# Optimization experiments

Hardware: AMD Instinct MI355X
Metric: run time of the kernel (lower is better)

The kernel has to match this reference:

```python
import jax, jax.numpy as jnp
import numpy as np

HEADS = 16
EMBED = 1024
HEAD_DIM = EMBED // HEADS


def setup_inputs() -> dict:
    key = jax.random.key(0)
    ks = jax.random.split(key, 10)
    B, SQ, SKV = 2, 2048, 2048
    s = 1.0 / np.sqrt(HEAD_DIM)
    sd = 1.0 / np.sqrt(EMBED)
    return {
        "queries": jax.random.normal(ks[0], (B, SQ, EMBED), jnp.float32),
        "values": jax.random.normal(ks[1], (B, SKV, EMBED), jnp.float32),
        "heads": HEADS,
        "Wv": jax.random.normal(ks[2], (HEAD_DIM, HEAD_DIM), jnp.float32) * s,
        "bv": jax.random.normal(ks[3], (HEAD_DIM,), jnp.float32) * 0.02,
        "Wk": jax.random.normal(ks[4], (HEAD_DIM, HEAD_DIM), jnp.float32) * s,
        "bk": jax.random.normal(ks[5], (HEAD_DIM,), jnp.float32) * 0.02,
        "Wq": jax.random.normal(ks[6], (HEAD_DIM, HEAD_DIM), jnp.float32) * s,
        "bq": jax.random.normal(ks[7], (HEAD_DIM,), jnp.float32) * 0.02,
        "Wd": jax.random.normal(ks[8], (EMBED, EMBED), jnp.float32) * sd,
        "bd": jax.random.normal(ks[9], (EMBED,), jnp.float32) * 0.02,
    }


def reference(queries, values, heads, Wv, bv, Wk, bk, Wq, bq, Wd, bd):
    n, sq, e = queries.shape
    skv = values.shape[1]
    d = e // heads
    # reshape to per-head layout [b, s, h, d]
    q_in = queries.reshape(n, sq, heads, d)
    v_in = values.reshape(n, skv, heads, d)
    # shared per-head linear projections (torch Linear: x @ W.T + b)
    v = jnp.einsum("bshd,ed->bshe", v_in, Wv) + bv
    # quirk preserved: keys computed from the ALREADY-PROJECTED values
    k = jnp.einsum("bshd,ed->bshe", v, Wk) + bk
    q = jnp.einsum("bshd,ed->bshe", q_in, Wq) + bq
    # full O(n^2) score matrix [b, h, sq, skv] (as in source)
    scores = jnp.einsum("bqhd,bkhd->bhqk", q, k) / jnp.sqrt(jnp.asarray(d, q.dtype))
    attn = jax.nn.softmax(scores, axis=-1)
    out = jnp.einsum("bhqk,bkhd->bqhd", attn, v).reshape(n, sq, e)
    return out @ Wd.T + bd
```

## Files before the change

### kernel.cpp

```cpp
#include <hip/hip_runtime.h>
#include <hip/hip_bf16.h>
#include <hip/hip_fp16.h>
#include <math.h>

typedef _Float16 f16;
typedef _Float16 f16x8 __attribute__((ext_vector_type(8)));
typedef _Float16 f16x4 __attribute__((ext_vector_type(4)));
typedef _Float16 f16x2 __attribute__((ext_vector_type(2)));
typedef unsigned short u16x8v __attribute__((ext_vector_type(8)));
typedef float f32x4 __attribute__((ext_vector_type(4)));

namespace {
constexpr int B = 2;
constexpr int H = 16;
constexpr int S = 2048;
constexpr int D = 64;
constexpr int E = 1024;
constexpr float QSCALE = 0.125f * 1.4426950408889634f;
}

#define GLOBAL_LOAD_LDS16(gp, lp)                                              \
  __builtin_amdgcn_global_load_lds(                                            \
      (const __attribute__((address_space(1))) void*)(gp),                     \
      (__attribute__((address_space(3))) void*)(lp), 16, 0, 0)

__global__ __launch_bounds__(256) void prep(const float* __restrict__ Wd, f16* __restrict__ wd16,
                                            const float* __restrict__ Wk, const float* __restrict__ Wv,
                                            const float* __restrict__ bv, const float* __restrict__ bk,
                                            float* __restrict__ Wkv, float* __restrict__ bkv) {
  if (blockIdx.x < 1024) {
    const int i = blockIdx.x * 256 + threadIdx.x;
    const float4 f = ((const float4*)Wd)[i];
    f16x4 o;
    o.x = (f16)f.x; o.y = (f16)f.y; o.z = (f16)f.z; o.w = (f16)f.w;
    *(f16x4*)(wd16 + 4 * (size_t)i) = o;
  } else {
    const int g = (blockIdx.x - 1024) * 256 + threadIdx.x;
    const int i = g >> 6, j = g & 63;
    float s = 0.f;
#pragma unroll 16
    for (int d = 0; d < 64; ++d) s = fmaf(Wk[i * 64 + d], Wv[d * 64 + j], s);
    Wkv[g] = s;
    if (g < 64) {
      float bb = bk[g];
#pragma unroll 16
      for (int d = 0; d < 64; ++d) bb = fmaf(Wk[g * 64 + d], bv[d], bb);
      bkv[g] = bb;
    }
  }
}

__global__ __launch_bounds__(256) void proj3_mfma(const float* __restrict__ xq,
                                                  const float* __restrict__ xv,
                                                  const float* __restrict__ Wq,
                                                  const float* __restrict__ bq,
                                                  const float* __restrict__ Wv,
                                                  const float* __restrict__ bv,
                                                  const float* __restrict__ Wkv,
                                                  const float* __restrict__ bkv,
                                                  f16* __restrict__ qp,
                                                  f16* __restrict__ vtp,
                                                  f16* __restrict__ kp) {
  __shared__ f16 tb[16 * 16 * 68];
  const int which = blockIdx.y;
  const float* x = which ? xv : xq;

  const int t = threadIdx.x, lane = t & 63, w = t >> 6;
  const int l15 = lane & 15, quad = lane >> 4;
  const int m0 = (blockIdx.x * 4 + w) * 64;

  f16x8 af[4][2];
#pragma unroll
  for (int mt = 0; mt < 4; ++mt)
#pragma unroll
    for (int kc = 0; kc < 2; ++kc) {
      const float* g = x + (size_t)(m0 + mt * 16 + l15) * 64 + kc * 32 + quad * 8;
      const float4 a = *(const float4*)g, b2 = *(const float4*)(g + 4);
      f16x8 v;
      v[0]=(f16)a.x; v[1]=(f16)a.y; v[2]=(f16)a.z; v[3]=(f16)a.w;
      v[4]=(f16)b2.x; v[5]=(f16)b2.y; v[6]=(f16)b2.z; v[7]=(f16)b2.w;
      af[mt][kc] = v;
    }

  const int npass = which ? 2 : 1;
  for (int pass = 0; pass < npass; ++pass) {
    const float* W    = which ? (pass ? Wkv : Wv) : Wq;
    const float* bias = which ? (pass ? bkv : bv) : bq;
    const bool vpass  = (which == 1) && (pass == 0);
    const bool kpass  = (which == 1) && (pass == 1);
    const float scale = which ? 1.0f : QSCALE;

    f16x8 wf[4][2];
#pragma unroll
    for (int nt = 0; nt < 4; ++nt)
#pragma unroll
      for (int kc = 0; kc < 2; ++kc) {
        const float* g = W + (size_t)(nt * 16 + l15) * 64 + kc * 32 + quad * 8;
        const float4 a = *(const float4*)g, b2 = *(const float4*)(g + 4);
        f16x8 v;
        v[0]=(f16)a.x; v[1]=(f16)a.y; v[2]=(f16)a.z; v[3]=(f16)a.w;
        v[4]=(f16)b2.x; v[5]=(f16)b2.y; v[6]=(f16)b2.z; v[7]=(f16)b2.w;
        wf[nt][kc] = v;
      }

    f32x4 acc[4][4];
#pragma unroll
    for (int nt = 0; nt < 4; ++nt)
#pragma unroll
      for (int mt = 0; mt < 4; ++mt) acc[nt][mt] = (f32x4){0.f, 0.f, 0.f, 0.f};
#pragma unroll
    for (int kc = 0; kc < 2; ++kc)
#pragma unroll
      for (int nt = 0; nt < 4; ++nt)
#pragma unroll
        for (int mt = 0; mt < 4; ++mt)
          acc[nt][mt] = __builtin_amdgcn_mfma_f32_16x16x32_f16(wf[nt][kc], af[mt][kc], acc[nt][mt], 0, 0, 0);

    float4 bl4[4];
#pragma unroll
    for (int nt = 0; nt < 4; ++nt) bl4[nt] = *(const float4*)&bias[nt * 16 + quad * 4];

#pragma unroll
    for (int mt = 0; mt < 4; ++mt) {
      const int g = m0 + mt * 16 + l15;
#pragma unroll
      for (int nt = 0; nt < 4; ++nt) {
        const float p0 = (acc[nt][mt][0] + bl4[nt].x) * scale;
        const float p1 = (acc[nt][mt][1] + bl4[nt].y) * scale;
        const float p2 = (acc[nt][mt][2] + bl4[nt].z) * scale;
        const float p3 = (acc[nt][mt][3] + bl4[nt].w) * scale;
        union { f16x4 v4; f16x2 hh[2]; } u;
        u.hh[0] = __builtin_bit_cast(f16x2, __builtin_amdgcn_cvt_pkrtz(p0, p1));
        u.hh[1] = __builtin_bit_cast(f16x2, __builtin_amdgcn_cvt_pkrtz(p2, p3));
        if (vpass) {
#pragma unroll
          for (int r = 0; r < 4; ++r)
            tb[(l15 * 64 + nt * 16 + quad * 4 + r) * 16 + w * 4 + mt] = u.v4[r];
        } else if (kpass) {
          *(f16x4*)&tb[(l15 * 16 + w * 4 + mt) * 68 + nt * 16 + quad * 4] = u.v4;
        } else {
          *(f16x4*)(qp + (size_t)g * 64 + nt * 16 + quad * 4) = u.v4;
        }
      }
    }

    if (vpass) {
      __syncthreads();
      const int bsb = blockIdx.x * 16;
      const int bb = bsb >> 11;
      const int sb = bsb & 2047;
      const int off = sb & 63;
      const int poff = (off & 32) | ((off & 16) >> 2);
      const int col0 = (sb - off) + poff;
#pragma unroll
      for (int k2 = 0; k2 < 4; ++k2) {
        const int pi = t * 4 + k2;
        const int h = pi >> 6, d = pi & 63;
        const f16x8 lo = *(const f16x8*)&tb[pi * 16];
        const f16x8 hi = *(const f16x8*)&tb[pi * 16 + 8];
        f16* orow = vtp + ((size_t)(bb * H + h) * 64 + d) * S + col0;
        f16x4 g0, g1, g2, g3;
#pragma unroll
        for (int j = 0; j < 4; ++j) { g0[j]=lo[j]; g1[j]=lo[4+j]; g2[j]=hi[j]; g3[j]=hi[4+j]; }
        *(f16x4*)(orow + 0)  = g0;
        *(f16x4*)(orow + 8)  = g1;
        *(f16x4*)(orow + 16) = g2;
        *(f16x4*)(orow + 24) = g3;
      }
      __syncthreads();
    } else if (kpass) {
      __syncthreads();
      const int bsb = blockIdx.x * 16;
      const int bb = bsb >> 11;
      const int sblk = bsb & 2047;
      const int h = t >> 4, sl = t & 15;
      f16* dst = kp + ((size_t)(bb * H + h) * S + sblk + sl) * 64;
      const f16* src = &tb[t * 68];
#pragma unroll
      for (int c = 0; c < 8; ++c)
        *(f16x8*)(dst + c * 8) = *(const f16x8*)(src + c * 8);
    }
  }
}

__global__ __launch_bounds__(256) void attn_mfma(const f16* __restrict__ qp,
                                                 const f16* __restrict__ kp,
                                                 const f16* __restrict__ vtp,
                                                 f16* __restrict__ ao) {
  __shared__ f16 ks[2][128 * 64];
  __shared__ f16 vs[2][64 * 128];
  const int t = threadIdx.x, lane = t & 63, w = t >> 6;
  const int l15 = lane & 15, quad = lane >> 4;
  const int bh = blockIdx.x;
  const int b = bh >> 4, h = bh & 15;
  const int q0 = blockIdx.y * 128;
  const f16* kbase = kp + (size_t)bh * S * D;
  const f16* vtbase = vtp + (size_t)bh * 64 * S;

  const int c1 = w * 64 + lane;
  const int krow = c1 >> 3;
  const size_t koff1 = (size_t)krow * D + (((c1 & 7) ^ (krow & 7)) * 8);
  const int vrow = c1 >> 4;
  const size_t voff1 = (size_t)vrow * S + (((c1 & 15) ^ (vrow & 15)) * 8);

  f16x8 qf[2][2];
#pragma unroll
  for (int mt = 0; mt < 2; ++mt)
#pragma unroll
    for (int kc = 0; kc < 2; ++kc)
      qf[mt][kc] = *(const f16x8*)(qp +
          ((size_t)(b * S + q0 + w * 32 + mt * 16 + l15) * H + h) * 64 + kc * 32 + quad * 8);

  f16x8 vb4;
#pragma unroll
  for (int j = 0; j < 8; ++j) vb4[j] = (l15 == 0) ? (f16)1.0f : (f16)0.0f;

  f32x4 O[2][5];
#pragma unroll
  for (int mt = 0; mt < 2; ++mt)
#pragma unroll
    for (int nt = 0; nt < 5; ++nt) O[mt][nt] = (f32x4){0.f, 0.f, 0.f, 0.f};

#define ISSUE_TILE(tt, buf)                                                    \
  {                                                                            \
    const f16* gk = kbase + (size_t)(tt) * (128 * D);                          \
    _Pragma("unroll")                                                          \
    for (int i = 0; i < 4; ++i)                                                \
      GLOBAL_LOAD_LDS16(gk + koff1 + (size_t)i * (32 * D),                     \
                        &ks[buf][(i * 256 + w * 64) * 8]);                     \
    const f16* gv = vtbase + (size_t)(tt) * 128;                               \
    _Pragma("unroll")                                                          \
    for (int i = 0; i < 4; ++i)                                                \
      GLOBAL_LOAD_LDS16(gv + voff1 + (size_t)i * (16 * S),                     \
                        &vs[buf][(i * 256 + w * 64) * 8]);                     \
  }

  ISSUE_TILE(0, 0);

  for (int kt = 0; kt < S / 128; ++kt) {
    const int rb = kt & 1;
    __asm__ volatile("s_waitcnt vmcnt(0)" ::: "memory");
    __builtin_amdgcn_s_barrier();
    __asm__ volatile("" ::: "memory");
    if (kt + 1 < S / 128) ISSUE_TILE(kt + 1, rb ^ 1);

#pragma unroll
    for (int kc = 0; kc < 4; ++kc) {
      f32x4 sc[2][2];
#pragma unroll
      for (int ntl = 0; ntl < 2; ++ntl)
#pragma unroll
        for (int mt = 0; mt < 2; ++mt) sc[ntl][mt] = (f32x4){0.f, 0.f, 0.f, 0.f};
      __builtin_amdgcn_s_setprio(1);
#pragma unroll
      for (int kcq = 0; kcq < 2; ++kcq)
#pragma unroll
        for (int ntl = 0; ntl < 2; ++ntl) {
          const int nt = kc * 2 + ntl;
          const f16x8 kf = *(const f16x8*)&ks[rb][(nt * 16 + l15) * 64 + (((kcq * 4 + quad) ^ (l15 & 7)) * 8)];
#pragma unroll
          for (int mt = 0; mt < 2; ++mt)
            sc[ntl][mt] = __builtin_amdgcn_mfma_f32_16x16x32_f16(kf, qf[mt][kcq], sc[ntl][mt], 0, 0, 0);
        }
      __builtin_amdgcn_s_setprio(0);

      f16x8 pa[2];
#pragma unroll
      for (int mt = 0; mt < 2; ++mt) {
        const f32x4 s0 = sc[0][mt], s1 = sc[1][mt];
        union { f16x8 v8; f16x2 hh[4]; } u;
        u.hh[0] = __builtin_bit_cast(f16x2, __builtin_amdgcn_cvt_pkrtz(
            __builtin_amdgcn_exp2f(s0[0]), __builtin_amdgcn_exp2f(s0[1])));
        u.hh[1] = __builtin_bit_cast(f16x2, __builtin_amdgcn_cvt_pkrtz(
            __builtin_amdgcn_exp2f(s0[2]), __builtin_amdgcn_exp2f(s0[3])));
        u.hh[2] = __builtin_bit_cast(f16x2, __builtin_amdgcn_cvt_pkrtz(
            __builtin_amdgcn_exp2f(s1[0]), __builtin_amdgcn_exp2f(s1[1])));
        u.hh[3] = __builtin_bit_cast(f16x2, __builtin_amdgcn_cvt_pkrtz(
            __builtin_amdgcn_exp2f(s1[2]), __builtin_amdgcn_exp2f(s1[3])));
        pa[mt] = u.v8;
      }

      __builtin_amdgcn_s_setprio(1);
#pragma unroll
      for (int nt = 0; nt < 4; ++nt) {
        const f16x8 vbf = *(const f16x8*)&vs[rb][(nt * 16 + l15) * 128 + (((kc * 4 + quad) ^ l15) * 8)];
#pragma unroll
        for (int mt = 0; mt < 2; ++mt)
          O[mt][nt] = __builtin_amdgcn_mfma_f32_16x16x32_f16(pa[mt], vbf, O[mt][nt], 0, 0, 0);
      }
#pragma unroll
      for (int mt = 0; mt < 2; ++mt)
        O[mt][4] = __builtin_amdgcn_mfma_f32_16x16x32_f16(pa[mt], vb4, O[mt][4], 0, 0, 0);
      __builtin_amdgcn_s_setprio(0);
    }
  }
#undef ISSUE_TILE

#pragma unroll
  for (int mt = 0; mt < 2; ++mt)
#pragma unroll
    for (int r = 0; r < 4; ++r) {
      const float l = __shfl(O[mt][4][r], quad << 4, 64);
      const float inv = 1.f / l;
      const int row = q0 + w * 32 + mt * 16 + quad * 4 + r;
      f16* o = ao + ((size_t)b * S + row) * E + h * D;
#pragma unroll
      for (int nt = 0; nt < 4; ++nt)
        o[nt * 16 + l15] = (f16)(O[mt][nt][r] * inv);
    }
}

__global__ __launch_bounds__(256) void dense_mfma(const f16* __restrict__ A,
                                                  const f16* __restrict__ Wd16,
                                                  const float* __restrict__ bd,
                                                  float* __restrict__ out) {
  __shared__ f16 as[3][128 * 64];
  __shared__ f16 bs[3][64 * 64];
  const int t = threadIdx.x;
  const int lane = t & 63;
  const int w = t >> 6;
  const int l15 = lane & 15;
  const int quad = lane >> 4;
  const int m0 = blockIdx.x * 128;
  const int n0 = blockIdx.y * 64;
  const int wm = (w >> 1) * 64, wn = (w & 1) * 32;

  const int srow = (lane >> 3);
  const int schunk = (lane & 7) ^ srow;
  const f16* ga0 = A    + (size_t)(m0 + w * 32 + srow) * E + schunk * 8;
  const f16* gb0 = Wd16 + (size_t)(n0 + w * 16 + srow) * E + schunk * 8;

  constexpr int NT = E / 64;

#define ISSUE_D(tt, ib)                                                        \
  {                                                                            \
    _Pragma("unroll")                                                          \
    for (int i = 0; i < 4; ++i)                                                \
      GLOBAL_LOAD_LDS16(ga0 + (size_t)(i * 8) * E + (tt) * 64,                 \
                        &as[ib][(w * 32 + i * 8) * 64]);                       \
    _Pragma("unroll")                                                          \
    for (int i = 0; i < 2; ++i)                                                \
      GLOBAL_LOAD_LDS16(gb0 + (size_t)(i * 8) * E + (tt) * 64,                 \
// ... 49 lines not shown
    for (int mt = 0; mt < 4; ++mt)
#pragma unroll
      for (int r = 0; r < 4; ++r)
        out[(size_t)(m0 + wm + mt * 16 + quad * 4 + r) * E + col] = acc[mt][nt][r] + bdv;
  }
}

extern "C" void kernel_launch(void* const* d_in, const int* in_sizes, int n_in,
                              void* d_out, int out_size, void* d_ws, size_t ws_size,
                              hipStream_t stream) {
  const float* queries = (const float*)d_in[0];
  const float* values  = (const float*)d_in[1];
  const float* Wv = (const float*)d_in[3];
  const float* bv = (const float*)d_in[4];
  const float* Wk = (const float*)d_in[5];
  const float* bk = (const float*)d_in[6];
  const float* Wq = (const float*)d_in[7];
  const float* bq = (const float*)d_in[8];
  const float* Wd = (const float*)d_in[9];
  const float* bd = (const float*)d_in[10];
  float* out = (float*)d_out;

  char* ws = (char*)d_ws;
  f16* qp    = (f16*)(ws);
  f16* kp    = (f16*)(ws + 8u * 1024 * 1024);
  f16* vtp   = (f16*)(ws + 16u * 1024 * 1024);
  f16* ao    = (f16*)(ws + 24u * 1024 * 1024);
  f16* wd16  = (f16*)(ws + 32u * 1024 * 1024);
  float* wkv = (float*)(ws + 34u * 1024 * 1024);
  float* bkv = (float*)(ws + 34u * 1024 * 1024 + 16384);
  (void)ws_size; (void)in_sizes; (void)n_in; (void)out_size;

  prep<<<1040, 256, 0, stream>>>(Wd, wd16, Wk, Wv, bv, bk, wkv, bkv);
  proj3_mfma<<<dim3(256, 2), 256, 0, stream>>>(queries, values, Wq, bq, Wv, bv, wkv, bkv, qp, vtp, kp);
  attn_mfma<<<dim3(B * H, S / 128), 256, 0, stream>>>(qp, kp, vtp, ao);
  dense_mfma<<<dim3(B * S / 128, E / 64), 256, 0, stream>>>(ao, wd16, bd, out);
}
```

Before: 177.7 us.

## Shrink attention tiles to 64 queries and 64 keys for higher occupancy

The attention kernel now uses 64-query blocks (16 rows per wave instead of 32) and 64-key tiles, halving LDS buffers and per-thread accumulators, and requests 4 blocks per CU via launch bounds. The grid doubles to 1024 blocks, which gives better CU fill and latency hiding on the device. In exchange, each K/V tile is reused by half as many queries, doubling global/L2 traffic for K and V, and there are twice as many barrier iterations per block.

```diff
diff --git a/kernel.cpp b/kernel.cpp
--- a/kernel.cpp
+++ b/kernel.cpp
@@ -183,74 +183,64 @@
   }
 }
 
-__global__ __launch_bounds__(256) void attn_mfma(const f16* __restrict__ qp,
-                                                 const f16* __restrict__ kp,
-                                                 const f16* __restrict__ vtp,
-                                                 f16* __restrict__ ao) {
-  __shared__ f16 ks[2][128 * 64];
-  __shared__ f16 vs[2][64 * 128];
+__global__ __launch_bounds__(256, 4) void attn_mfma(const f16* __restrict__ qp,
+                                                    const f16* __restrict__ kp,
+                                                    const f16* __restrict__ vtp,
+                                                    f16* __restrict__ ao) {
+  __shared__ f16 ks[2][64 * 64];
+  __shared__ f16 vs[2][64 * 64];
   const int t = threadIdx.x, lane = t & 63, w = t >> 6;
   const int l15 = lane & 15, quad = lane >> 4;
   const int bh = blockIdx.x;
   const int b = bh >> 4, h = bh & 15;
-  const int q0 = blockIdx.y * 128;
+  const int q0 = blockIdx.y * 64;
   const f16* kbase = kp + (size_t)bh * S * D;
   const f16* vtbase = vtp + (size_t)bh * 64 * S;
 
-  const int c1 = w * 64 + lane;
-  const int krow = c1 >> 3;
-  const size_t koff1 = (size_t)krow * D + (((c1 & 7) ^ (krow & 7)) * 8);
-  const int vrow = c1 >> 4;
-  const size_t voff1 = (size_t)vrow * S + (((c1 & 15) ^ (vrow & 15)) * 8);
-
-  f16x8 qf[2][2];
-#pragma unroll
-  for (int mt = 0; mt < 2; ++mt)
-#pragma unroll
-    for (int kc = 0; kc < 2; ++kc)
-      qf[mt][kc] = *(const f16x8*)(qp +
-          ((size_t)(b * S + q0 + w * 32 + mt * 16 + l15) * H + h) * 64 + kc * 32 + quad * 8);
+  const int row1 = t >> 3;
+  const size_t koff1 = (size_t)row1 * D + (((t & 7) ^ (row1 & 7)) * 8);
+  const size_t koff2 = koff1 + (size_t)32 * D;
+  const size_t voff1 = (size_t)row1 * S + (((t & 7) ^ (row1 & 7)) * 8);
+  const size_t voff2 = voff1 + (size_t)32 * S;
+
+  f16x8 qf[2];
+#pragma unroll
+  for (int kc = 0; kc < 2; ++kc)
+    qf[kc] = *(const f16x8*)(qp +
+        ((size_t)(b * S + q0 + w * 16 + l15) * H + h) * 64 + kc * 32 + quad * 8);
 
   f16x8 vb4;
 #pragma unroll
   for (int j = 0; j < 8; ++j) vb4[j] = (l15 == 0) ? (f16)1.0f : (f16)0.0f;
 
-  f32x4 O[2][5];
-#pragma unroll
-  for (int mt = 0; mt < 2; ++mt)
-#pragma unroll
-    for (int nt = 0; nt < 5; ++nt) O[mt][nt] = (f32x4){0.f, 0.f, 0.f, 0.f};
+  f32x4 O[5];
+#pragma unroll
+  for (int nt = 0; nt < 5; ++nt) O[nt] = (f32x4){0.f, 0.f, 0.f, 0.f};
 
 #define ISSUE_TILE(tt, buf)                                                    \
   {                                                                            \
-    const f16* gk = kbase + (size_t)(tt) * (128 * D);                          \
-    _Pragma("unroll")                                                          \
-    for (int i = 0; i < 4; ++i)                                                \
-      GLOBAL_LOAD_LDS16(gk + koff1 + (size_t)i * (32 * D),                     \
-                        &ks[buf][(i * 256 + w * 64) * 8]);                     \
-    const f16* gv = vtbase + (size_t)(tt) * 128;                               \
-    _Pragma("unroll")                                                          \
-    for (int i = 0; i < 4; ++i)                                                \
-      GLOBAL_LOAD_LDS16(gv + voff1 + (size_t)i * (16 * S),                     \
-                        &vs[buf][(i * 256 + w * 64) * 8]);                     \
+    const f16* gk = kbase + (size_t)(tt) * (64 * D);                           \
+    GLOBAL_LOAD_LDS16(gk + koff1, &ks[buf][t * 8]);                            \
+    GLOBAL_LOAD_LDS16(gk + koff2, &ks[buf][(t + 256) * 8]);                    \
+    const f16* gv = vtbase + (size_t)(tt) * 64;                                \
+    GLOBAL_LOAD_LDS16(gv + voff1, &vs[buf][t * 8]);                            \
+    GLOBAL_LOAD_LDS16(gv + voff2, &vs[buf][(t + 256) * 8]);                    \
   }
 
   ISSUE_TILE(0, 0);
 
-  for (int kt = 0; kt < S / 128; ++kt) {
+  for (int kt = 0; kt < S / 64; ++kt) {
     const int rb = kt & 1;
     __asm__ volatile("s_waitcnt vmcnt(0)" ::: "memory");
     __builtin_amdgcn_s_barrier();
     __asm__ volatile("" ::: "memory");
-    if (kt + 1 < S / 128) ISSUE_TILE(kt + 1, rb ^ 1);
-
-#pragma unroll
-    for (int kc = 0; kc < 4; ++kc) {
-      f32x4 sc[2][2];
-#pragma unroll
-      for (int ntl = 0; ntl < 2; ++ntl)
-#pragma unroll
-        for (int mt = 0; mt < 2; ++mt) sc[ntl][mt] = (f32x4){0.f, 0.f, 0.f, 0.f};
+    if (kt + 1 < S / 64) ISSUE_TILE(kt + 1, rb ^ 1);
+
+#pragma unroll
+    for (int kc = 0; kc < 2; ++kc) {
+      f32x4 sc[2];
+#pragma unroll
+      for (int ntl = 0; ntl < 2; ++ntl) sc[ntl] = (f32x4){0.f, 0.f, 0.f, 0.f};
       __builtin_amdgcn_s_setprio(1);
 #pragma unroll
       for (int kcq = 0; kcq < 2; ++kcq)
@@ -258,16 +248,13 @@
         for (int ntl = 0; ntl < 2; ++ntl) {
           const int nt = kc * 2 + ntl;
           const f16x8 kf = *(const f16x8*)&ks[rb][(nt * 16 + l15) * 64 + (((kcq * 4 + quad) ^ (l15 & 7)) * 8)];
-#pragma unroll
-          for (int mt = 0; mt < 2; ++mt)
-            sc[ntl][mt] = __builtin_amdgcn_mfma_f32_16x16x32_f16(kf, qf[mt][kcq], sc[ntl][mt], 0, 0, 0);
+          sc[ntl] = __builtin_amdgcn_mfma_f32_16x16x32_f16(kf, qf[kcq], sc[ntl], 0, 0, 0);
         }
       __builtin_amdgcn_s_setprio(0);
 
-      f16x8 pa[2];
-#pragma unroll
-      for (int mt = 0; mt < 2; ++mt) {
-        const f32x4 s0 = sc[0][mt], s1 = sc[1][mt];
+      f16x8 pa;
+      {
+        const f32x4 s0 = sc[0], s1 = sc[1];
         union { f16x8 v8; f16x2 hh[4]; } u;
         u.hh[0] = __builtin_bit_cast(f16x2, __builtin_amdgcn_cvt_pkrtz(
             __builtin_amdgcn_exp2f(s0[0]), __builtin_amdgcn_exp2f(s0[1])));
@@ -277,37 +264,31 @@
             __builtin_amdgcn_exp2f(s1[0]), __builtin_amdgcn_exp2f(s1[1])));
         u.hh[3] = __builtin_bit_cast(f16x2, __builtin_amdgcn_cvt_pkrtz(
             __builtin_amdgcn_exp2f(s1[2]), __builtin_amdgcn_exp2f(s1[3])));
-        pa[mt] = u.v8;
+        pa = u.v8;
       }
 
       __builtin_amdgcn_s_setprio(1);
 #pragma unroll
       for (int nt = 0; nt < 4; ++nt) {
-        const f16x8 vbf = *(const f16x8*)&vs[rb][(nt * 16 + l15) * 128 + (((kc * 4 + quad) ^ l15) * 8)];
-#pragma unroll
-        for (int mt = 0; mt < 2; ++mt)
-          O[mt][nt] = __builtin_amdgcn_mfma_f32_16x16x32_f16(pa[mt], vbf, O[mt][nt], 0, 0, 0);
-      }
-#pragma unroll
-      for (int mt = 0; mt < 2; ++mt)
-        O[mt][4] = __builtin_amdgcn_mfma_f32_16x16x32_f16(pa[mt], vb4, O[mt][4], 0, 0, 0);
+        const f16x8 vbf = *(const f16x8*)&vs[rb][(nt * 16 + l15) * 64 + (((kc * 4 + quad) ^ (l15 & 7)) * 8)];
+        O[nt] = __builtin_amdgcn_mfma_f32_16x16x32_f16(pa, vbf, O[nt], 0, 0, 0);
+      }
+      O[4] = __builtin_amdgcn_mfma_f32_16x16x32_f16(pa, vb4, O[4], 0, 0, 0);
       __builtin_amdgcn_s_setprio(0);
     }
   }
 #undef ISSUE_TILE
 
 #pragma unroll
-  for (int mt = 0; mt < 2; ++mt)
-#pragma unroll
-    for (int r = 0; r < 4; ++r) {
-      const float l = __shfl(O[mt][4][r], quad << 4, 64);
-      const float inv = 1.f / l;
-      const int row = q0 + w * 32 + mt * 16 + quad * 4 + r;
-      f16* o = ao + ((size_t)b * S + row) * E + h * D;
-#pragma unroll
-      for (int nt = 0; nt < 4; ++nt)
-        o[nt * 16 + l15] = (f16)(O[mt][nt][r] * inv);
-    }
+  for (int r = 0; r < 4; ++r) {
+    const float l = __shfl(O[4][r], quad << 4, 64);
+    const float inv = 1.f / l;
+    const int row = q0 + w * 16 + quad * 4 + r;
+    f16* o = ao + ((size_t)b * S + row) * E + h * D;
+#pragma unroll
+    for (int nt = 0; nt < 4; ++nt)
+      o[nt * 16 + l15] = (f16)(O[nt][r] * inv);
+  }
 }
 
 __global__ __launch_bounds__(256) void dense_mfma(const f16* __restrict__ A,
@@ -424,6 +405,6 @@
 
   prep<<<1040, 256, 0, stream>>>(Wd, wd16, Wk, Wv, bv, bk, wkv, bkv);
   proj3_mfma<<<dim3(256, 2), 256, 0, stream>>>(queries, values, Wq, bq, Wv, bv, wkv, bkv, qp, vtp, kp);
-  attn_mfma<<<dim3(B * H, S / 128), 256, 0, stream>>>(qp, kp, vtp, ao);
+  attn_mfma<<<dim3(B * H, S / 64), 256, 0, stream>>>(qp, kp, vtp, ao);
   dense_mfma<<<dim3(B * S / 128, E / 64), 256, 0, stream>>>(ao, wd16, bd, out);
 }
```

Result: no change. 180.6 us (+1.7%).

## Split KV across waves in attention and move V projection to its own kernel

Applied to the files above, without the earlier changes.

The attention kernel now uses 64-query blocks, twice as many blocks, and splits each 64-key tile across two wave pairs. Partial O and row-sum accumulators are combined through shared memory at the end. The V-transpose projection moves out of the fused projection kernel into a separate per-head kernel, leaving Q/K projection with a single pass. The aim is better occupancy and parallelism on the dominant attention stage, at the cost of an extra kernel launch and a final cross-wave reduction.

```diff
diff --git a/kernel.cpp b/kernel.cpp
--- a/kernel.cpp
+++ b/kernel.cpp
@@ -50,20 +50,20 @@
   }
 }
 
-__global__ __launch_bounds__(256) void proj3_mfma(const float* __restrict__ xq,
-                                                  const float* __restrict__ xv,
-                                                  const float* __restrict__ Wq,
-                                                  const float* __restrict__ bq,
-                                                  const float* __restrict__ Wv,
-                                                  const float* __restrict__ bv,
-                                                  const float* __restrict__ Wkv,
-                                                  const float* __restrict__ bkv,
-                                                  f16* __restrict__ qp,
-                                                  f16* __restrict__ vtp,
-                                                  f16* __restrict__ kp) {
+__global__ __launch_bounds__(256) void projqk_mfma(const float* __restrict__ xq,
+                                                   const float* __restrict__ xv,
+                                                   const float* __restrict__ Wq,
+                                                   const float* __restrict__ bq,
+                                                   const float* __restrict__ Wkv,
+                                                   const float* __restrict__ bkv,
+                                                   f16* __restrict__ qp,
+                                                   f16* __restrict__ kp) {
   __shared__ f16 tb[16 * 16 * 68];
   const int which = blockIdx.y;
-  const float* x = which ? xv : xq;
+  const float* x    = which ? xv : xq;
+  const float* W    = which ? Wkv : Wq;
+  const float* bias = which ? bkv : bq;
+  const float scale = which ? 1.0f : QSCALE;
 
   const int t = threadIdx.x, lane = t & 63, w = t >> 6;
   const int l15 = lane & 15, quad = lane >> 4;
@@ -82,126 +82,153 @@
       af[mt][kc] = v;
     }
 
-  const int npass = which ? 2 : 1;
-  for (int pass = 0; pass < npass; ++pass) {
-    const float* W    = which ? (pass ? Wkv : Wv) : Wq;
-    const float* bias = which ? (pass ? bkv : bv) : bq;
-    const bool vpass  = (which == 1) && (pass == 0);
-    const bool kpass  = (which == 1) && (pass == 1);
-    const float scale = which ? 1.0f : QSCALE;
-
-    f16x8 wf[4][2];
+  f16x8 wf[4][2];
+#pragma unroll
+  for (int nt = 0; nt < 4; ++nt)
+#pragma unroll
+    for (int kc = 0; kc < 2; ++kc) {
+      const float* g = W + (size_t)(nt * 16 + l15) * 64 + kc * 32 + quad * 8;
+      const float4 a = *(const float4*)g, b2 = *(const float4*)(g + 4);
+      f16x8 v;
+      v[0]=(f16)a.x; v[1]=(f16)a.y; v[2]=(f16)a.z; v[3]=(f16)a.w;
+      v[4]=(f16)b2.x; v[5]=(f16)b2.y; v[6]=(f16)b2.z; v[7]=(f16)b2.w;
+      wf[nt][kc] = v;
+    }
+
+  f32x4 acc[4][4];
+#pragma unroll
+  for (int nt = 0; nt < 4; ++nt)
+#pragma unroll
+    for (int mt = 0; mt < 4; ++mt) acc[nt][mt] = (f32x4){0.f, 0.f, 0.f, 0.f};
+#pragma unroll
+  for (int kc = 0; kc < 2; ++kc)
 #pragma unroll
     for (int nt = 0; nt < 4; ++nt)
 #pragma unroll
-      for (int kc = 0; kc < 2; ++kc) {
-        const float* g = W + (size_t)(nt * 16 + l15) * 64 + kc * 32 + quad * 8;
-        const float4 a = *(const float4*)g, b2 = *(const float4*)(g + 4);
-        f16x8 v;
-        v[0]=(f16)a.x; v[1]=(f16)a.y; v[2]=(f16)a.z; v[3]=(f16)a.w;
-        v[4]=(f16)b2.x; v[5]=(f16)b2.y; v[6]=(f16)b2.z; v[7]=(f16)b2.w;
-        wf[nt][kc] = v;
+      for (int mt = 0; mt < 4; ++mt)
+        acc[nt][mt] = __builtin_amdgcn_mfma_f32_16x16x32_f16(wf[nt][kc], af[mt][kc], acc[nt][mt], 0, 0, 0);
+
+  float4 bl4[4];
+#pragma unroll
+  for (int nt = 0; nt < 4; ++nt) bl4[nt] = *(const float4*)&bias[nt * 16 + quad * 4];
+
+#pragma unroll
+  for (int mt = 0; mt < 4; ++mt) {
+    const int g = m0 + mt * 16 + l15;
+#pragma unroll
+    for (int nt = 0; nt < 4; ++nt) {
+      const float p0 = (acc[nt][mt][0] + bl4[nt].x) * scale;
+      const float p1 = (acc[nt][mt][1] + bl4[nt].y) * scale;
+      const float p2 = (acc[nt][mt][2] + bl4[nt].z) * scale;
+      const float p3 = (acc[nt][mt][3] + bl4[nt].w) * scale;
+      union { f16x4 v4; f16x2 hh[2]; } u;
+      u.hh[0] = __builtin_bit_cast(f16x2, __builtin_amdgcn_cvt_pkrtz(p0, p1));
+      u.hh[1] = __builtin_bit_cast(f16x2, __builtin_amdgcn_cvt_pkrtz(p2, p3));
+      if (which) {
+        *(f16x4*)&tb[(l15 * 16 + w * 4 + mt) * 68 + nt * 16 + quad * 4] = u.v4;
+      } else {
+        *(f16x4*)(qp + (size_t)g * 64 + nt * 16 + quad * 4) = u.v4;
       }
-
-    f32x4 acc[4][4];
-#pragma unroll
-    for (int nt = 0; nt < 4; ++nt)
-#pragma unroll
-      for (int mt = 0; mt < 4; ++mt) acc[nt][mt] = (f32x4){0.f, 0.f, 0.f, 0.f};
-#pragma unroll
-    for (int kc = 0; kc < 2; ++kc)
-#pragma unroll
-      for (int nt = 0; nt < 4; ++nt)
-#pragma unroll
-        for (int mt = 0; mt < 4; ++mt)
-          acc[nt][mt] = __builtin_amdgcn_mfma_f32_16x16x32_f16(wf[nt][kc], af[mt][kc], acc[nt][mt], 0, 0, 0);
-
-    float4 bl4[4];
-#pragma unroll
-    for (int nt = 0; nt < 4; ++nt) bl4[nt] = *(const float4*)&bias[nt * 16 + quad * 4];
-
-#pragma unroll
-    for (int mt = 0; mt < 4; ++mt) {
-      const int g = m0 + mt * 16 + l15;
-#pragma unroll
-      for (int nt = 0; nt < 4; ++nt) {
-        const float p0 = (acc[nt][mt][0] + bl4[nt].x) * scale;
-        const float p1 = (acc[nt][mt][1] + bl4[nt].y) * scale;
-        const float p2 = (acc[nt][mt][2] + bl4[nt].z) * scale;
-        const float p3 = (acc[nt][mt][3] + bl4[nt].w) * scale;
-        union { f16x4 v4; f16x2 hh[2]; } u;
-        u.hh[0] = __builtin_bit_cast(f16x2, __builtin_amdgcn_cvt_pkrtz(p0, p1));
-        u.hh[1] = __builtin_bit_cast(f16x2, __builtin_amdgcn_cvt_pkrtz(p2, p3));
-        if (vpass) {
-#pragma unroll
-          for (int r = 0; r < 4; ++r)
-            tb[(l15 * 64 + nt * 16 + quad * 4 + r) * 16 + w * 4 + mt] = u.v4[r];
-        } else if (kpass) {
-          *(f16x4*)&tb[(l15 * 16 + w * 4 + mt) * 68 + nt * 16 + quad * 4] = u.v4;
-        } else {
-          *(f16x4*)(qp + (size_t)g * 64 + nt * 16 + quad * 4) = u.v4;
-        }
-      }
-    }
-
-    if (vpass) {
-      __syncthreads();
-      const int bsb = blockIdx.x * 16;
-      const int bb = bsb >> 11;
-      const int sb = bsb & 2047;
-      const int off = sb & 63;
-      const int poff = (off & 32) | ((off & 16) >> 2);
-      const int col0 = (sb - off) + poff;
-#pragma unroll
-      for (int k2 = 0; k2 < 4; ++k2) {
-        const int pi = t * 4 + k2;
-        const int h = pi >> 6, d = pi & 63;
-        const f16x8 lo = *(const f16x8*)&tb[pi * 16];
-        const f16x8 hi = *(const f16x8*)&tb[pi * 16 + 8];
-        f16* orow = vtp + ((size_t)(bb * H + h) * 64 + d) * S + col0;
-        f16x4 g0, g1, g2, g3;
-#pragma unroll
-        for (int j = 0; j < 4; ++j) { g0[j]=lo[j]; g1[j]=lo[4+j]; g2[j]=hi[j]; g3[j]=hi[4+j]; }
-        *(f16x4*)(orow + 0)  = g0;
-        *(f16x4*)(orow + 8)  = g1;
-        *(f16x4*)(orow + 16) = g2;
-        *(f16x4*)(orow + 24) = g3;
-      }
-      __syncthreads();
-    } else if (kpass) {
-      __syncthreads();
-      const int bsb = blockIdx.x * 16;
-      const int bb = bsb >> 11;
-      const int sblk = bsb & 2047;
-      const int h = t >> 4, sl = t & 15;
-      f16* dst = kp + ((size_t)(bb * H + h) * S + sblk + sl) * 64;
-      const f16* src = &tb[t * 68];
-#pragma unroll
-      for (int c = 0; c < 8; ++c)
-        *(f16x8*)(dst + c * 8) = *(const f16x8*)(src + c * 8);
-    }
-  }
-}
-
-__global__ __launch_bounds__(256) void attn_mfma(const f16* __restrict__ qp,
-                                                 const f16* __restrict__ kp,
-                                                 const f16* __restrict__ vtp,
-                                                 f16* __restrict__ ao) {
-  __shared__ f16 ks[2][128 * 64];
-  __shared__ f16 vs[2][64 * 128];
+    }
+  }
+
+  if (which) {
+    __syncthreads();
+    const int bsb = blockIdx.x * 16;
+    const int bb = bsb >> 11;
+    const int sblk = bsb & 2047;
+    const int h = t >> 4, sl = t & 15;
+    f16* dst = kp + ((size_t)(bb * H + h) * S + sblk + sl) * 64;
+    const f16* src = &tb[t * 68];
+#pragma unroll
+    for (int c = 0; c < 8; ++c)
+      *(f16x8*)(dst + c * 8) = *(const f16x8*)(src + c * 8);
+  }
+}
+
+__global__ __launch_bounds__(256) void projv_mfma(const float* __restrict__ xv,
+                                                  const float* __restrict__ Wv,
+                                                  const float* __restrict__ bv,
+                                                  f16* __restrict__ vtp) {
+  __shared__ f16 tb[64 * 72];
   const int t = threadIdx.x, lane = t & 63, w = t >> 6;
   const int l15 = lane & 15, quad = lane >> 4;
+  const int b = blockIdx.x >> 5, s0 = (blockIdx.x & 31) * 64;
+  const int h = blockIdx.y;
+
+  f16x8 af[2];
+#pragma unroll
+  for (int kc = 0; kc < 2; ++kc) {
+    const float* g = xv + ((size_t)(b * S + s0 + w * 16 + l15) * H + h) * 64 + kc * 32 + quad * 8;
+    const float4 a = *(const float4*)g, b2 = *(const float4*)(g + 4);
+    f16x8 v;
+    v[0]=(f16)a.x; v[1]=(f16)a.y; v[2]=(f16)a.z; v[3]=(f16)a.w;
+    v[4]=(f16)b2.x; v[5]=(f16)b2.y; v[6]=(f16)b2.z; v[7]=(f16)b2.w;
+    af[kc] = v;
+  }
+  f16x8 wf[4][2];
+#pragma unroll
+  for (int nt = 0; nt < 4; ++nt)
+#pragma unroll
+    for (int kc = 0; kc < 2; ++kc) {
+      const float* g = Wv + (size_t)(nt * 16 + l15) * 64 + kc * 32 + quad * 8;
+      const float4 a = *(const float4*)g, b2 = *(const float4*)(g + 4);
+      f16x8 v;
+      v[0]=(f16)a.x; v[1]=(f16)a.y; v[2]=(f16)a.z; v[3]=(f16)a.w;
+      v[4]=(f16)b2.x; v[5]=(f16)b2.y; v[6]=(f16)b2.z; v[7]=(f16)b2.w;
+      wf[nt][kc] = v;
+    }
+
+  f32x4 acc[4];
+#pragma unroll
+  for (int nt = 0; nt < 4; ++nt) acc[nt] = (f32x4){0.f, 0.f, 0.f, 0.f};
+#pragma unroll
+  for (int kc = 0; kc < 2; ++kc)
+#pragma unroll
+    for (int nt = 0; nt < 4; ++nt)
+      acc[nt] = __builtin_amdgcn_mfma_f32_16x16x32_f16(af[kc], wf[nt][kc], acc[nt], 0, 0, 0);
+
+  float bl[4];
+#pragma unroll
+  for (int nt = 0; nt < 4; ++nt) bl[nt] = bv[nt * 16 + l15];
+
+#pragma unroll
+  for (int nt = 0; nt < 4; ++nt)
+#pragma unroll
+    for (int r = 0; r < 4; ++r)
+      tb[(nt * 16 + l15) * 72 + w * 16 + quad * 4 + r] = (f16)(acc[nt][r] + bl[nt]);
+
+  __syncthreads();
+  const int d = t >> 2;
+  f16* orow = vtp + ((size_t)(b * H + h) * 64 + d) * S + s0;
+  const f16* src = &tb[d * 72];
+#pragma unroll
+  for (int j = 0; j < 4; ++j) {
+    const int g = (t & 3) * 4 + j;
+    const int p = ((g >> 3) & 1) * 32 + ((g >> 1) & 1) * 16 + (g & 1) * 8 + ((g >> 2) & 1) * 4;
+    *(f16x4*)(orow + p) = *(const f16x4*)(src + g * 4);
+  }
+}
+
+__global__ __launch_bounds__(256, 4) void attn_mfma(const f16* __restrict__ qp,
+                                                    const f16* __restrict__ kp,
+                                                    const f16* __restrict__ vtp,
+                                                    f16* __restrict__ ao) {
+  __shared__ f16 smem[4][64 * 64];
+  const int t = threadIdx.x, lane = t & 63, w = t >> 6;
+  const int l15 = lane & 15, quad = lane >> 4;
+  const int wq = w >> 1, wk = w & 1;
   const int bh = blockIdx.x;
   const int b = bh >> 4, h = bh & 15;
-  const int q0 = blockIdx.y * 128;
+  const int q0 = blockIdx.y * 64;
   const f16* kbase = kp + (size_t)bh * S * D;
   const f16* vtbase = vtp + (size_t)bh * 64 * S;
 
-  const int c1 = w * 64 + lane;
-  const int krow = c1 >> 3;
-  const size_t koff1 = (size_t)krow * D + (((c1 & 7) ^ (krow & 7)) * 8);
-  const int vrow = c1 >> 4;
-  const size_t voff1 = (size_t)vrow * S + (((c1 & 15) ^ (vrow & 15)) * 8);
+  const int row1 = t >> 3;
+  const size_t koff1 = (size_t)row1 * D + (((t & 7) ^ (row1 & 7)) * 8);
+  const size_t koff2 = koff1 + (size_t)32 * D;
+  const size_t voff1 = (size_t)row1 * S + (((t & 7) ^ (row1 & 7)) * 8);
+  const size_t voff2 = voff1 + (size_t)32 * S;
 
   f16x8 qf[2][2];
 #pragma unroll
@@ -209,7 +236,7 @@
 #pragma unroll
     for (int kc = 0; kc < 2; ++kc)
       qf[mt][kc] = *(const f16x8*)(qp +
-          ((size_t)(b * S + q0 + w * 32 + mt * 16 + l15) * H + h) * 64 + kc * 32 + quad * 8);
+          ((size_t)(b * S + q0 + wq * 32 + mt * 16 + l15) * H + h) * 64 + kc * 32 + quad * 8);
 
   f16x8 vb4;
 #pragma unroll
@@ -223,91 +250,104 @@
 
 #define ISSUE_TILE(tt, buf)                                                    \
   {                                                                            \
-    const f16* gk = kbase + (size_t)(tt) * (128 * D);                          \
-    _Pragma("unroll")                                                          \
-    for (int i = 0; i < 4; ++i)                                                \
-      GLOBAL_LOAD_LDS16(gk + koff1 + (size_t)i * (32 * D),                     \
-                        &ks[buf][(i * 256 + w * 64) * 8]);                     \
-    const f16* gv = vtbase + (size_t)(tt) * 128;                               \
-    _Pragma("unroll")                                                          \
-    for (int i = 0; i < 4; ++i)                                                \
-      GLOBAL_LOAD_LDS16(gv + voff1 + (size_t)i * (16 * S),                     \
-                        &vs[buf][(i * 256 + w * 64) * 8]);                     \
+    const f16* gk = kbase + (size_t)(tt) * (64 * D);                           \
+    GLOBAL_LOAD_LDS16(gk + koff1, &smem[buf][t * 8]);                          \
+    GLOBAL_LOAD_LDS16(gk + koff2, &smem[buf][(t + 256) * 8]);                  \
+    const f16* gv = vtbase + (size_t)(tt) * 64;                                \
+    GLOBAL_LOAD_LDS16(gv + voff1, &smem[2 + (buf)][t * 8]);                    \
+    GLOBAL_LOAD_LDS16(gv + voff2, &smem[2 + (buf)][(t + 256) * 8]);            \
   }
 
   ISSUE_TILE(0, 0);
 
-  for (int kt = 0; kt < S / 128; ++kt) {
+  for (int kt = 0; kt < S / 64; ++kt) {
     const int rb = kt & 1;
     __asm__ volatile("s_waitcnt vmcnt(0)" ::: "memory");
     __builtin_amdgcn_s_barrier();
     __asm__ volatile("" ::: "memory");
-    if (kt + 1 < S / 128) ISSUE_TILE(kt + 1, rb ^ 1);
-
-#pragma unroll
-    for (int kc = 0; kc < 4; ++kc) {
-      f32x4 sc[2][2];
-#pragma unroll
-      for (int ntl = 0; ntl < 2; ++ntl)
-#pragma unroll
-        for (int mt = 0; mt < 2; ++mt) sc[ntl][mt] = (f32x4){0.f, 0.f, 0.f, 0.f};
-      __builtin_amdgcn_s_setprio(1);
-#pragma unroll
-      for (int kcq = 0; kcq < 2; ++kcq)
-#pragma unroll
-        for (int ntl = 0; ntl < 2; ++ntl) {
-          const int nt = kc * 2 + ntl;
-          const f16x8 kf = *(const f16x8*)&ks[rb][(nt * 16 + l15) * 64 + (((kcq * 4 + quad) ^ (l15 & 7)) * 8)];
-#pragma unroll
-          for (int mt = 0; mt < 2; ++mt)
-            sc[ntl][mt] = __builtin_amdgcn_mfma_f32_16x16x32_f16(kf, qf[mt][kcq], sc[ntl][mt], 0, 0, 0);
-        }
-      __builtin_amdgcn_s_setprio(0);
-
-      f16x8 pa[2];
-#pragma unroll
-      for (int mt = 0; mt < 2; ++mt) {
-        const f32x4 s0 = sc[0][mt], s1 = sc[1][mt];
-        union { f16x8 v8; f16x2 hh[4]; } u;
-        u.hh[0] = __builtin_bit_cast(f16x2, __builtin_amdgcn_cvt_pkrtz(
-            __builtin_amdgcn_exp2f(s0[0]), __builtin_amdgcn_exp2f(s0[1])));
-        u.hh[1] = __builtin_bit_cast(f16x2, __builtin_amdgcn_cvt_pkrtz(
-            __builtin_amdgcn_exp2f(s0[2]), __builtin_amdgcn_exp2f(s0[3])));
-        u.hh[2] = __builtin_bit_cast(f16x2, __builtin_amdgcn_cvt_pkrtz(
-            __builtin_amdgcn_exp2f(s1[0]), __builtin_amdgcn_exp2f(s1[1])));
-        u.hh[3] = __builtin_bit_cast(f16x2, __builtin_amdgcn_cvt_pkrtz(
-            __builtin_amdgcn_exp2f(s1[2]), __builtin_amdgcn_exp2f(s1[3])));
-        pa[mt] = u.v8;
+    if (kt + 1 < S / 64) ISSUE_TILE(kt + 1, rb ^ 1);
+
+    f32x4 sc[2][2];
+#pragma unroll
+    for (int ntl = 0; ntl < 2; ++ntl)
+#pragma unroll
+      for (int mt = 0; mt < 2; ++mt) sc[ntl][mt] = (f32x4){0.f, 0.f, 0.f, 0.f};
+    __builtin_amdgcn_s_setprio(1);
+#pragma unroll
+    for (int kcq = 0; kcq < 2; ++kcq)
+#pragma unroll
+      for (int ntl = 0; ntl < 2; ++ntl) {
+        const f16x8 kf = *(const f16x8*)&smem[rb][(wk * 32 + ntl * 16 + l15) * 64 + (((kcq * 4 + quad) ^ (l15 & 7)) * 8)];
+#pragma unroll
+        for (int mt = 0; mt < 2; ++mt)
+          sc[ntl][mt] = __builtin_amdgcn_mfma_f32_16x16x32_f16(kf, qf[mt][kcq], sc[ntl][mt], 0, 0, 0);
       }
-
-      __builtin_amdgcn_s_setprio(1);
-#pragma unroll
-      for (int nt = 0; nt < 4; ++nt) {
-        const f16x8 vbf = *(const f16x8*)&vs[rb][(nt * 16 + l15) * 128 + (((kc * 4 + quad) ^ l15) * 8)];
-#pragma unroll
-        for (int mt = 0; mt < 2; ++mt)
-          O[mt][nt] = __builtin_amdgcn_mfma_f32_16x16x32_f16(pa[mt], vbf, O[mt][nt], 0, 0, 0);
+    __builtin_amdgcn_s_setprio(0);
+
+    f16x8 pa[2];
+#pragma unroll
+    for (int mt = 0; mt < 2; ++mt) {
+      const f32x4 s0 = sc[0][mt], s1 = sc[1][mt];
+      union { f16x8 v8; f16x2 hh[4]; } u;
+      u.hh[0] = __builtin_bit_cast(f16x2, __builtin_amdgcn_cvt_pkrtz(
+          __builtin_amdgcn_exp2f(s0[0]), __builtin_amdgcn_exp2f(s0[1])));
+      u.hh[1] = __builtin_bit_cast(f16x2, __builtin_amdgcn_cvt_pkrtz(
+          __builtin_amdgcn_exp2f(s0[2]), __builtin_amdgcn_exp2f(s0[3])));
+      u.hh[2] = __builtin_bit_cast(f16x2, __builtin_amdgcn_cvt_pkrtz(
+          __builtin_amdgcn_exp2f(s1[0]), __builtin_amdgcn_exp2f(s1[1])));
+      u.hh[3] = __builtin_bit_cast(f16x2, __builtin_amdgcn_cvt_pkrtz(
+          __builtin_amdgcn_exp2f(s1[2]), __builtin_amdgcn_exp2f(s1[3])));
+      pa[mt] = u.v8;
+    }
+
+    __builtin_amdgcn_s_setprio(1);
+#pragma unroll
+    for (int nt = 0; nt < 4; ++nt) {
+      const f16x8 vbf = *(const f16x8*)&smem[2 + rb][(nt * 16 + l15) * 64 + (((wk * 4 + quad) ^ (l15 & 7)) * 8)];
+#pragma unroll
+      for (int mt = 0; mt < 2; ++mt)
+        O[mt][nt] = __builtin_amdgcn_mfma_f32_16x16x32_f16(pa[mt], vbf, O[mt][nt], 0, 0, 0);
+    }
+#pragma unroll
+    for (int mt = 0; mt < 2; ++mt)
+      O[mt][4] = __builtin_amdgcn_mfma_f32_16x16x32_f16(pa[mt], vb4, O[mt][4], 0, 0, 0);
+    __builtin_amdgcn_s_setprio(0);
+  }
+#undef ISSUE_TILE
+
+  __syncthreads();
+  float* red = (float*)&smem[0][0];
+  if (wk) {
+    float* dst = red + (size_t)(wq * 64 + lane) * 41;
+#pragma unroll
+    for (int mt = 0; mt < 2; ++mt)
+#pragma unroll
+      for (int nt = 0; nt < 5; ++nt)
+#pragma unroll
+        for (int r = 0; r < 4; ++r) dst[mt * 20 + nt * 4 + r] = O[mt][nt][r];
+  }
+  __syncthreads();
+  if (!wk) {
+    const float* src = red + (size_t)(wq * 64 + lane) * 41;
+#pragma unroll
+    for (int mt = 0; mt < 2; ++mt)
+#pragma unroll
+      for (int nt = 0; nt < 5; ++nt)
+#pragma unroll
+        for (int r = 0; r < 4; ++r) O[mt][nt][r] += src[mt * 20 + nt * 4 + r];
+#pragma unroll
+    for (int mt = 0; mt < 2; ++mt)
+#pragma unroll
+      for (int r = 0; r < 4; ++r) {
+        const float l = __shfl(O[mt][4][r], quad << 4, 64);
+        const float inv = 1.f / l;
+        const int row = q0 + wq * 32 + mt * 16 + quad * 4 + r;
+        f16* o = ao + ((size_t)b * S + row) * E + h * D;
+#pragma unroll
+        for (int nt = 0; nt < 4; ++nt)
+          o[nt * 16 + l15] = (f16)(O[mt][nt][r] * inv);
       }
-#pragma unroll
-      for (int mt = 0; mt < 2; ++mt)
-        O[mt][4] = __builtin_amdgcn_mfma_f32_16x16x32_f16(pa[mt], vb4, O[mt][4], 0, 0, 0);
-      __builtin_amdgcn_s_setprio(0);
-    }
-  }
-#undef ISSUE_TILE
-
-#pragma unroll
-  for (int mt = 0; mt < 2; ++mt)
-#pragma unroll
-    for (int r = 0; r < 4; ++r) {
-      const float l = __shfl(O[mt][4][r], quad << 4, 64);
-      const float inv = 1.f / l;
-      const int row = q0 + w * 32 + mt * 16 + quad * 4 + r;
-      f16* o = ao + ((size_t)b * S + row) * E + h * D;
-#pragma unroll
-      for (int nt = 0; nt < 4; ++nt)
-        o[nt * 16 + l15] = (f16)(O[mt][nt][r] * inv);
-    }
+  }
 }
 
 __global__ __launch_bounds__(256) void dense_mfma(const f16* __restrict__ A,
@@ -423,7 +463,8 @@
   (void)ws_size; (void)in_sizes; (void)n_in; (void)out_size;
 
   prep<<<1040, 256, 0, stream>>>(Wd, wd16, Wk, Wv, bv, bk, wkv, bkv);
-  proj3_mfma<<<dim3(256, 2), 256, 0, stream>>>(queries, values, Wq, bq, Wv, bv, wkv, bkv, qp, vtp, kp);
-  attn_mfma<<<dim3(B * H, S / 128), 256, 0, stream>>>(qp, kp, vtp, ao);
+  projqk_mfma<<<dim3(256, 2), 256, 0, stream>>>(queries, values, Wq, bq, wkv, bkv, qp, kp);
+  projv_mfma<<<dim3(B * S / 64, H), 256, 0, stream>>>(values, Wv, bv, vtp);
+  attn_mfma<<<dim3(B * H, S / 64), 256, 0, stream>>>(qp, kp, vtp, ao);
   dense_mfma<<<dim3(B * S / 128, E / 64), 256, 0, stream>>>(ao, wd16, bd, out);
 }
```

New measurement: 179.3 us. Within noise of the previous version (+0.9%).

## Split attention KV dimension across wave pairs with LDS reduction, 512 threads

Applied to the files above, without the earlier changes.

The attention kernel now uses 512 threads per block. Each pair of waves shares a 32-row query slab and splits each 64-key tile between them, so each block runs 8 waves. The KV tile shrinks from 128 to 64 keys to cut LDS to 32 KB, allowing more blocks per CU. Partial O and row-sum accumulators are combined through LDS at the end, which adds a few barriers and extra LDS traffic. The aim is more waves in flight to hide latency, at the cost of twice as many loop iterations and barriers.

```diff
diff --git a/kernel.cpp b/kernel.cpp
--- a/kernel.cpp
+++ b/kernel.cpp
@@ -183,25 +183,23 @@
   }
 }
 
-__global__ __launch_bounds__(256) void attn_mfma(const f16* __restrict__ qp,
-                                                 const f16* __restrict__ kp,
-                                                 const f16* __restrict__ vtp,
-                                                 f16* __restrict__ ao) {
-  __shared__ f16 ks[2][128 * 64];
-  __shared__ f16 vs[2][64 * 128];
+__global__ __launch_bounds__(512, 4) void attn_mfma(const f16* __restrict__ qp,
+                                                    const f16* __restrict__ kp,
+                                                    const f16* __restrict__ vtp,
+                                                    f16* __restrict__ ao) {
+  __shared__ f16 smem[4][64 * 64];
   const int t = threadIdx.x, lane = t & 63, w = t >> 6;
   const int l15 = lane & 15, quad = lane >> 4;
+  const int wq = w >> 1, wk = w & 1;
   const int bh = blockIdx.x;
   const int b = bh >> 4, h = bh & 15;
   const int q0 = blockIdx.y * 128;
   const f16* kbase = kp + (size_t)bh * S * D;
   const f16* vtbase = vtp + (size_t)bh * 64 * S;
 
-  const int c1 = w * 64 + lane;
-  const int krow = c1 >> 3;
-  const size_t koff1 = (size_t)krow * D + (((c1 & 7) ^ (krow & 7)) * 8);
-  const int vrow = c1 >> 4;
-  const size_t voff1 = (size_t)vrow * S + (((c1 & 15) ^ (vrow & 15)) * 8);
+  const int row1 = t >> 3;
+  const size_t koff = (size_t)row1 * D + (((t & 7) ^ (row1 & 7)) * 8);
+  const size_t voff = (size_t)row1 * S + (((t & 7) ^ (row1 & 7)) * 8);
 
   f16x8 qf[2][2];
 #pragma unroll
@@ -209,7 +207,7 @@
 #pragma unroll
     for (int kc = 0; kc < 2; ++kc)
       qf[mt][kc] = *(const f16x8*)(qp +
-          ((size_t)(b * S + q0 + w * 32 + mt * 16 + l15) * H + h) * 64 + kc * 32 + quad * 8);
+          ((size_t)(b * S + q0 + wq * 32 + mt * 16 + l15) * H + h) * 64 + kc * 32 + quad * 8);
 
   f16x8 vb4;
 #pragma unroll
@@ -223,91 +221,115 @@
 
 #define ISSUE_TILE(tt, buf)                                                    \
   {                                                                            \
-    const f16* gk = kbase + (size_t)(tt) * (128 * D);                          \
-    _Pragma("unroll")                                                          \
-    for (int i = 0; i < 4; ++i)                                                \
-      GLOBAL_LOAD_LDS16(gk + koff1 + (size_t)i * (32 * D),                     \
-                        &ks[buf][(i * 256 + w * 64) * 8]);                     \
-    const f16* gv = vtbase + (size_t)(tt) * 128;                               \
-    _Pragma("unroll")                                                          \
-    for (int i = 0; i < 4; ++i)                                                \
-      GLOBAL_LOAD_LDS16(gv + voff1 + (size_t)i * (16 * S),                     \
-                        &vs[buf][(i * 256 + w * 64) * 8]);                     \
+    const f16* gk = kbase + (size_t)(tt) * (64 * D);                           \
+    GLOBAL_LOAD_LDS16(gk + koff, &smem[buf][t * 8]);                           \
+    const f16* gv = vtbase + (size_t)(tt) * 64;                                \
+    GLOBAL_LOAD_LDS16(gv + voff, &smem[2 + (buf)][t * 8]);                     \
   }
 
   ISSUE_TILE(0, 0);
 
-  for (int kt = 0; kt < S / 128; ++kt) {
+  for (int kt = 0; kt < S / 64; ++kt) {
     const int rb = kt & 1;
     __asm__ volatile("s_waitcnt vmcnt(0)" ::: "memory");
     __builtin_amdgcn_s_barrier();
     __asm__ volatile("" ::: "memory");
-    if (kt + 1 < S / 128) ISSUE_TILE(kt + 1, rb ^ 1);
-
-#pragma unroll
-    for (int kc = 0; kc < 4; ++kc) {
-      f32x4 sc[2][2];
-#pragma unroll
-      for (int ntl = 0; ntl < 2; ++ntl)
-#pragma unroll
-        for (int mt = 0; mt < 2; ++mt) sc[ntl][mt] = (f32x4){0.f, 0.f, 0.f, 0.f};
-      __builtin_amdgcn_s_setprio(1);
-#pragma unroll
-      for (int kcq = 0; kcq < 2; ++kcq)
-#pragma unroll
-        for (int ntl = 0; ntl < 2; ++ntl) {
-          const int nt = kc * 2 + ntl;
-          const f16x8 kf = *(const f16x8*)&ks[rb][(nt * 16 + l15) * 64 + (((kcq * 4 + quad) ^ (l15 & 7)) * 8)];
-#pragma unroll
-          for (int mt = 0; mt < 2; ++mt)
-            sc[ntl][mt] = __builtin_amdgcn_mfma_f32_16x16x32_f16(kf, qf[mt][kcq], sc[ntl][mt], 0, 0, 0);
-        }
-      __builtin_amdgcn_s_setprio(0);
-
-      f16x8 pa[2];
-#pragma unroll
-      for (int mt = 0; mt < 2; ++mt) {
-        const f32x4 s0 = sc[0][mt], s1 = sc[1][mt];
-        union { f16x8 v8; f16x2 hh[4]; } u;
-        u.hh[0] = __builtin_bit_cast(f16x2, __builtin_amdgcn_cvt_pkrtz(
-            __builtin_amdgcn_exp2f(s0[0]), __builtin_amdgcn_exp2f(s0[1])));
-        u.hh[1] = __builtin_bit_cast(f16x2, __builtin_amdgcn_cvt_pkrtz(
-            __builtin_amdgcn_exp2f(s0[2]), __builtin_amdgcn_exp2f(s0[3])));
-        u.hh[2] = __builtin_bit_cast(f16x2, __builtin_amdgcn_cvt_pkrtz(
-            __builtin_amdgcn_exp2f(s1[0]), __builtin_amdgcn_exp2f(s1[1])));
-        u.hh[3] = __builtin_bit_cast(f16x2, __builtin_amdgcn_cvt_pkrtz(
-            __builtin_amdgcn_exp2f(s1[2]), __builtin_amdgcn_exp2f(s1[3])));
-        pa[mt] = u.v8;
-      }
-
-      __builtin_amdgcn_s_setprio(1);
-#pragma unroll
-      for (int nt = 0; nt < 4; ++nt) {
-        const f16x8 vbf = *(const f16x8*)&vs[rb][(nt * 16 + l15) * 128 + (((kc * 4 + quad) ^ l15) * 8)];
+    if (kt + 1 < S / 64) ISSUE_TILE(kt + 1, rb ^ 1);
+
+    f32x4 sc[2][2];
+#pragma unroll
+    for (int ntl = 0; ntl < 2; ++ntl)
+#pragma unroll
+      for (int mt = 0; mt < 2; ++mt) sc[ntl][mt] = (f32x4){0.f, 0.f, 0.f, 0.f};
+    __builtin_amdgcn_s_setprio(1);
+#pragma unroll
+    for (int kcq = 0; kcq < 2; ++kcq)
+#pragma unroll
+      for (int ntl = 0; ntl < 2; ++ntl) {
+        const f16x8 kf = *(const f16x8*)&smem[rb][(wk * 32 + ntl * 16 + l15) * 64 + (((kcq * 4 + quad) ^ (l15 & 7)) * 8)];
 #pragma unroll
         for (int mt = 0; mt < 2; ++mt)
-          O[mt][nt] = __builtin_amdgcn_mfma_f32_16x16x32_f16(pa[mt], vbf, O[mt][nt], 0, 0, 0);
-      }
+          sc[ntl][mt] = __builtin_amdgcn_mfma_f32_16x16x32_f16(kf, qf[mt][kcq], sc[ntl][mt], 0, 0, 0);
+      }
+    __builtin_amdgcn_s_setprio(0);
+
+    f16x8 pa[2];
+#pragma unroll
+    for (int mt = 0; mt < 2; ++mt) {
+      const f32x4 s0 = sc[0][mt], s1 = sc[1][mt];
+      union { f16x8 v8; f16x2 hh[4]; } u;
+      u.hh[0] = __builtin_bit_cast(f16x2, __builtin_amdgcn_cvt_pkrtz(
+          __builtin_amdgcn_exp2f(s0[0]), __builtin_amdgcn_exp2f(s0[1])));
+      u.hh[1] = __builtin_bit_cast(f16x2, __builtin_amdgcn_cvt_pkrtz(
+          __builtin_amdgcn_exp2f(s0[2]), __builtin_amdgcn_exp2f(s0[3])));
+      u.hh[2] = __builtin_bit_cast(f16x2, __builtin_amdgcn_cvt_pkrtz(
+          __builtin_amdgcn_exp2f(s1[0]), __builtin_amdgcn_exp2f(s1[1])));
+      u.hh[3] = __builtin_bit_cast(f16x2, __builtin_amdgcn_cvt_pkrtz(
+          __builtin_amdgcn_exp2f(s1[2]), __builtin_amdgcn_exp2f(s1[3])));
+      pa[mt] = u.v8;
+    }
+
+    __builtin_amdgcn_s_setprio(1);
+#pragma unroll
+    for (int nt = 0; nt < 4; ++nt) {
+      const f16x8 vbf = *(const f16x8*)&smem[2 + rb][(nt * 16 + l15) * 64 + (((wk * 4 + quad) ^ (l15 & 7)) * 8)];
 #pragma unroll
       for (int mt = 0; mt < 2; ++mt)
-        O[mt][4] = __builtin_amdgcn_mfma_f32_16x16x32_f16(pa[mt], vb4, O[mt][4], 0, 0, 0);
-      __builtin_amdgcn_s_setprio(0);
-    }
+        O[mt][nt] = __builtin_amdgcn_mfma_f32_16x16x32_f16(pa[mt], vbf, O[mt][nt], 0, 0, 0);
+    }
+#pragma unroll
+    for (int mt = 0; mt < 2; ++mt)
+      O[mt][4] = __builtin_amdgcn_mfma_f32_16x16x32_f16(pa[mt], vb4, O[mt][4], 0, 0, 0);
+    __builtin_amdgcn_s_setprio(0);
   }
 #undef ISSUE_TILE
 
-#pragma unroll
-  for (int mt = 0; mt < 2; ++mt)
-#pragma unroll
-    for (int r = 0; r < 4; ++r) {
-      const float l = __shfl(O[mt][4][r], quad << 4, 64);
-      const float inv = 1.f / l;
-      const int row = q0 + w * 32 + mt * 16 + quad * 4 + r;
-      f16* o = ao + ((size_t)b * S + row) * E + h * D;
-#pragma unroll
-      for (int nt = 0; nt < 4; ++nt)
-        o[nt * 16 + l15] = (f16)(O[mt][nt][r] * inv);
-    }
+  float* red = (float*)&smem[0][0];
+  __syncthreads();
+  if (wk) {
+    float* dst = red + (size_t)(wq * 64 + lane) * 20;
+#pragma unroll
+    for (int nt = 0; nt < 5; ++nt)
+#pragma unroll
+      for (int r = 0; r < 4; ++r) dst[nt * 4 + r] = O[0][nt][r];
+  }
+  __syncthreads();
+  if (!wk) {
+    const float* src = red + (size_t)(wq * 64 + lane) * 20;
+#pragma unroll
+    for (int nt = 0; nt < 5; ++nt)
+#pragma unroll
+      for (int r = 0; r < 4; ++r) O[0][nt][r] += src[nt * 4 + r];
+  }
+  __syncthreads();
+  if (wk) {
+    float* dst = red + (size_t)(wq * 64 + lane) * 20;
+#pragma unroll
+    for (int nt = 0; nt < 5; ++nt)
+#pragma unroll
+      for (int r = 0; r < 4; ++r) dst[nt * 4 + r] = O[1][nt][r];
+  }
+  __syncthreads();
+  if (!wk) {
+    const float* src = red + (size_t)(wq * 64 + lane) * 20;
+#pragma unroll
+    for (int nt = 0; nt < 5; ++nt)
+#pragma unroll
+      for (int r = 0; r < 4; ++r) O[1][nt][r] += src[nt * 4 + r];
+
+#pragma unroll
+    for (int mt = 0; mt < 2; ++mt)
+#pragma unroll
+      for (int r = 0; r < 4; ++r) {
+        const float l = __shfl(O[mt][4][r], quad << 4, 64);
+        const float inv = 1.f / l;
+        const int row = q0 + wq * 32 + mt * 16 + quad * 4 + r;
+        f16* o = ao + ((size_t)b * S + row) * E + h * D;
+#pragma unroll
+        for (int nt = 0; nt < 4; ++nt)
+          o[nt * 16 + l15] = (f16)(O[mt][nt][r] * inv);
+      }
+  }
 }
 
 __global__ __launch_bounds__(256) void dense_mfma(const f16* __restrict__ A,
@@ -424,6 +446,6 @@
 
   prep<<<1040, 256, 0, stream>>>(Wd, wd16, Wk, Wv, bv, bk, wkv, bkv);
   proj3_mfma<<<dim3(256, 2), 256, 0, stream>>>(queries, values, Wq, bq, Wv, bv, wkv, bkv, qp, vtp, kp);
-  attn_mfma<<<dim3(B * H, S / 128), 256, 0, stream>>>(qp, kp, vtp, ao);
+  attn_mfma<<<dim3(B * H, S / 128), 512, 0, stream>>>(qp, kp, vtp, ao);
   dense_mfma<<<dim3(B * S / 128, E / 64), 256, 0, stream>>>(ao, wd16, bd, out);
 }
```

Result: no change. 175.5 us (-1.2%).
